# Kernel tuning notes

Measured on AMD Instinct MI355X. Metric: run time of the kernel, lower is better.

## Reference

```python
import jax, jax.numpy as jnp
import numpy as np

INPUT_SIZE = 128
HIDDEN = 256
BATCH = 64
SEQ = 2048


def setup_inputs() -> dict:
    key = jax.random.key(0)
    k1, k2, k3, k4, k5 = jax.random.split(key, 5)
    bound = 1.0 / np.sqrt(HIDDEN)
    x = jax.random.normal(k1, (BATCH, SEQ, INPUT_SIZE), dtype=jnp.float32)
    W_ih = jax.random.uniform(k2, (4 * HIDDEN, INPUT_SIZE), minval=-bound, maxval=bound, dtype=jnp.float32)
    W_hh = jax.random.uniform(k3, (4 * HIDDEN, HIDDEN), minval=-bound, maxval=bound, dtype=jnp.float32)
    b_ih = jax.random.uniform(k4, (4 * HIDDEN,), minval=-bound, maxval=bound, dtype=jnp.float32)
    b_hh = jax.random.uniform(k5, (4 * HIDDEN,), minval=-bound, maxval=bound, dtype=jnp.float32)
    return {"x": x, "W_ih": W_ih, "W_hh": W_hh, "b_ih": b_ih, "b_hh": b_hh}


def reference(x, W_ih, W_hh, b_ih, b_hh):
    # Faithful to the source: lstm_cell is called WITHOUT previous state at every
    # step, so h_prev = c_prev = 0 for each timestep. W_hh @ h_prev == 0, and
    # f_gate * c_prev == 0. Each timestep is independent -> vectorize over time.
    H = W_hh.shape[1]
    # gates: [B, T, 4H]
    gates = jnp.einsum('bti,gi->btg', x, W_ih) + b_ih + b_hh
    i_g, f_g, g_g, o_g = jnp.split(gates, 4, axis=-1)  # PyTorch order: i, f, g, o
    i_g = jax.nn.sigmoid(i_g)
    g_g = jnp.tanh(g_g)
    o_g = jax.nn.sigmoid(o_g)
    c = i_g * g_g                      # f_g * c_prev == 0 since c_prev = 0
    h = o_g * jnp.tanh(c)
    return (h, c)
```

## Files before the change

### kernel.cpp

```cpp
#include <hip/hip_runtime.h>
#include <hip/hip_bf16.h>
#include <stdint.h>


#define M_TOTAL   (64 * 2048)
#define K_DIM     128
#define N_OUT     256
#define TILE_ROWS 64
#define TILE_BYTES (TILE_ROWS * K_DIM * 4)
#define NBLK      256
#define ITERS     (M_TOTAL / TILE_ROWS / NBLK)

typedef __bf16 bf16x8 __attribute__((ext_vector_type(8)));
typedef float  f32x16 __attribute__((ext_vector_type(16)));

static __device__ __forceinline__ bf16x8 cvt8(float4 a, float4 b) {
    bf16x8 r;
    r[0] = (__bf16)a.x; r[1] = (__bf16)a.y; r[2] = (__bf16)a.z; r[3] = (__bf16)a.w;
    r[4] = (__bf16)b.x; r[5] = (__bf16)b.y; r[6] = (__bf16)b.z; r[7] = (__bf16)b.w;
    return r;
}

static __device__ __forceinline__ float fast_sigmoid(float x) {
    float e = __expf(-x);
    return __builtin_amdgcn_rcpf(1.0f + e);
}

static __device__ __forceinline__ float fast_tanh(float x) {
    float e = __expf(2.0f * x);
    return 1.0f - 2.0f * __builtin_amdgcn_rcpf(e + 1.0f);
}

static __device__ __forceinline__ void gload_lds16(const void* g, void* l) {
    __builtin_amdgcn_global_load_lds(
        (const __attribute__((address_space(1))) void*)g,
        (__attribute__((address_space(3))) void*)l, 16, 0, 0);
}

__global__ __launch_bounds__(512, 1)
void lstm_gates_kernel(const float* __restrict__ x,
                       const float* __restrict__ Wih,
                       const float* __restrict__ bih,
                       const float* __restrict__ bhh,
                       float* __restrict__ hout,
                       float* __restrict__ cout)
{
    __shared__ uint8_t lds[3 * TILE_BYTES];

    const int tid   = threadIdx.x;
    const int lane  = tid & 63;
    const int w     = tid >> 6;
    const int c0    = w * 32;
    const int ln31  = lane & 31;
    const int khalf = (lane >> 5) * 8;
    const uint32_t xr = (uint32_t)(ln31 & 7) << 4;

    bf16x8 bi[8], bg[8], bo[8];
    {
        const float4* wi = (const float4*)(Wih + (size_t)(0   + c0 + ln31) * K_DIM + khalf);
        const float4* wg = (const float4*)(Wih + (size_t)(512 + c0 + ln31) * K_DIM + khalf);
        const float4* wo = (const float4*)(Wih + (size_t)(768 + c0 + ln31) * K_DIM + khalf);
        #pragma unroll
        for (int kk = 0; kk < 8; ++kk) {
            bi[kk] = cvt8(wi[kk * 4], wi[kk * 4 + 1]);
            bg[kk] = cvt8(wg[kk * 4], wg[kk * 4 + 1]);
            bo[kk] = cvt8(wo[kk * 4], wo[kk * 4 + 1]);
        }
    }
    const float bias_i = bih[0   + c0 + ln31] + bhh[0   + c0 + ln31];
    const float bias_g = bih[512 + c0 + ln31] + bhh[512 + c0 + ln31];
    const float bias_o = bih[768 + c0 + ln31] + bhh[768 + c0 + ln31];

    const int t0 = blockIdx.x * ITERS;

    auto stage = [&](int buf, int t) {
        const uint8_t* gbase = (const uint8_t*)x + (size_t)t * TILE_BYTES;
        uint8_t* lbase = lds + (size_t)buf * TILE_BYTES + (size_t)w * 4096;
        #pragma unroll
        for (int j = 0; j < 4; ++j) {
            uint32_t d   = (uint32_t)w * 4096u + (uint32_t)j * 1024u + (uint32_t)lane * 16u;
            uint32_t src = d ^ (((d >> 9) & 7u) << 4);
            gload_lds16(gbase + src, lbase + (uint32_t)j * 1024u);
        }
    };

    auto compute = [&](int buf, int t) {
        const uint8_t* lbase = lds + (size_t)buf * TILE_BYTES;
        #pragma unroll
        for (int s = 0; s < 2; ++s) {
            const uint8_t* rowp = lbase + (uint32_t)(s * 32 + ln31) * 512u;
            bf16x8 a[8];
            #pragma unroll
            for (int kk = 0; kk < 8; ++kk) {
                const uint32_t off0 = (uint32_t)khalf * 4u + (uint32_t)kk * 64u;
                float4 lo = *(const float4*)(rowp + ((off0      ) ^ xr));
                float4 hi = *(const float4*)(rowp + ((off0 + 16u) ^ xr));
                a[kk] = cvt8(lo, hi);
            }
            f32x16 ai = (f32x16)0.0f, ag = (f32x16)0.0f, ao = (f32x16)0.0f;
            #pragma unroll
            for (int kk = 0; kk < 8; ++kk) {
                ai = __builtin_amdgcn_mfma_f32_32x32x16_bf16(a[kk], bi[kk], ai, 0, 0, 0);
                ag = __builtin_amdgcn_mfma_f32_32x32x16_bf16(a[kk], bg[kk], ag, 0, 0, 0);
                ao = __builtin_amdgcn_mfma_f32_32x32x16_bf16(a[kk], bo[kk], ao, 0, 0, 0);
            }
            const int m0 = t * TILE_ROWS + s * 32;
            #pragma unroll
            for (int r = 0; r < 16; ++r) {
                const int row = m0 + (r & 3) + 8 * (r >> 2) + 4 * (lane >> 5);
                float vi = ai[r] + bias_i;
                float vg = ag[r] + bias_g;
                float vo = ao[r] + bias_o;
                float si = fast_sigmoid(vi);
                float tg = fast_tanh(vg);
                float so = fast_sigmoid(vo);
                float c  = si * tg;
                float tc = fast_tanh(c);
                float h  = so * tc;
                const size_t off = (size_t)row * N_OUT + c0 + ln31;
                hout[off] = h;
                cout[off] = c;
            }
        }
    };

    stage(0, t0);
    for (int i = 0; i < ITERS; ++i) {
        __syncthreads();
        if (i + 1 < ITERS) stage((i + 1) % 3, t0 + i + 1);
        compute(i % 3, t0 + i);
    }
}

extern "C" void kernel_launch(void* const* d_in, const int* in_sizes, int n_in,
                              void* d_out, int out_size, void* d_ws, size_t ws_size,
                              hipStream_t stream) {
    const float* x   = (const float*)d_in[0];
    const float* Wih = (const float*)d_in[1];
    const float* bih = (const float*)d_in[3];
    const float* bhh = (const float*)d_in[4];
    float* hout = (float*)d_out;
    float* cout = hout + (size_t)M_TOTAL * N_OUT;

    lstm_gates_kernel<<<NBLK, 512, 0, stream>>>(x, Wih, bih, bhh, hout, cout);
}
```

Baseline: 341.7 us.

## Use 16x16 MFMA tiles with 1024-thread blocks and double-buffered LDS

Switches from 32x32x16 to 16x16x32 bf16 MFMA, so each of 16 waves now owns 16 output columns instead of 32. Block size doubles to 1024 threads, and the LDS ring drops from three buffers to two to fit the larger block. The aim is more resident waves to hide global-load and store latency, and smaller accumulators to cut register pressure. The cost is narrower 64-byte row segments per output store and less slack in the double-buffered pipeline.

```diff
diff --git a/kernel.cpp b/kernel.cpp
--- a/kernel.cpp
+++ b/kernel.cpp
@@ -12,7 +12,7 @@
 #define ITERS     (M_TOTAL / TILE_ROWS / NBLK)
 
 typedef __bf16 bf16x8 __attribute__((ext_vector_type(8)));
-typedef float  f32x16 __attribute__((ext_vector_type(16)));
+typedef float  f32x4  __attribute__((ext_vector_type(4)));
 
 static __device__ __forceinline__ bf16x8 cvt8(float4 a, float4 b) {
     bf16x8 r;
@@ -37,7 +37,7 @@
         (__attribute__((address_space(3))) void*)l, 16, 0, 0);
 }
 
-__global__ __launch_bounds__(512, 1)
+__global__ __launch_bounds__(1024, 4)
 void lstm_gates_kernel(const float* __restrict__ x,
                        const float* __restrict__ Wih,
                        const float* __restrict__ bih,
@@ -45,40 +45,39 @@
                        float* __restrict__ hout,
                        float* __restrict__ cout)
 {
-    __shared__ uint8_t lds[3 * TILE_BYTES];
+    __shared__ uint8_t lds[2 * TILE_BYTES];
 
-    const int tid   = threadIdx.x;
-    const int lane  = tid & 63;
-    const int w     = tid >> 6;
-    const int c0    = w * 32;
-    const int ln31  = lane & 31;
-    const int khalf = (lane >> 5) * 8;
-    const uint32_t xr = (uint32_t)(ln31 & 7) << 4;
+    const int tid  = threadIdx.x;
+    const int lane = tid & 63;
+    const int w    = tid >> 6;
+    const int c0   = w * 16;
+    const int r15  = lane & 15;
+    const int q    = lane >> 4;
 
-    bf16x8 bi[8], bg[8], bo[8];
+    bf16x8 bi[4], bg[4], bo[4];
     {
-        const float4* wi = (const float4*)(Wih + (size_t)(0   + c0 + ln31) * K_DIM + khalf);
-        const float4* wg = (const float4*)(Wih + (size_t)(512 + c0 + ln31) * K_DIM + khalf);
-        const float4* wo = (const float4*)(Wih + (size_t)(768 + c0 + ln31) * K_DIM + khalf);
+        const float* wi = Wih + (size_t)(0   + c0 + r15) * K_DIM + q * 8;
+        const float* wg = Wih + (size_t)(512 + c0 + r15) * K_DIM + q * 8;
+        const float* wo = Wih + (size_t)(768 + c0 + r15) * K_DIM + q * 8;
         #pragma unroll
-        for (int kk = 0; kk < 8; ++kk) {
-            bi[kk] = cvt8(wi[kk * 4], wi[kk * 4 + 1]);
-            bg[kk] = cvt8(wg[kk * 4], wg[kk * 4 + 1]);
-            bo[kk] = cvt8(wo[kk * 4], wo[kk * 4 + 1]);
+        for (int kk = 0; kk < 4; ++kk) {
+            bi[kk] = cvt8(*(const float4*)(wi + kk * 32), *(const float4*)(wi + kk * 32 + 4));
+            bg[kk] = cvt8(*(const float4*)(wg + kk * 32), *(const float4*)(wg + kk * 32 + 4));
+            bo[kk] = cvt8(*(const float4*)(wo + kk * 32), *(const float4*)(wo + kk * 32 + 4));
         }
     }
-    const float bias_i = bih[0   + c0 + ln31] + bhh[0   + c0 + ln31];
-    const float bias_g = bih[512 + c0 + ln31] + bhh[512 + c0 + ln31];
-    const float bias_o = bih[768 + c0 + ln31] + bhh[768 + c0 + ln31];
+    const float bias_i = bih[0   + c0 + r15] + bhh[0   + c0 + r15];
+    const float bias_g = bih[512 + c0 + r15] + bhh[512 + c0 + r15];
+    const float bias_o = bih[768 + c0 + r15] + bhh[768 + c0 + r15];
 
     const int t0 = blockIdx.x * ITERS;
 
     auto stage = [&](int buf, int t) {
         const uint8_t* gbase = (const uint8_t*)x + (size_t)t * TILE_BYTES;
-        uint8_t* lbase = lds + (size_t)buf * TILE_BYTES + (size_t)w * 4096;
+        uint8_t* lbase = lds + (size_t)buf * TILE_BYTES + (size_t)w * 2048;
         #pragma unroll
-        for (int j = 0; j < 4; ++j) {
-            uint32_t d   = (uint32_t)w * 4096u + (uint32_t)j * 1024u + (uint32_t)lane * 16u;
+        for (int j = 0; j < 2; ++j) {
+            uint32_t d   = (uint32_t)w * 2048u + (uint32_t)j * 1024u + (uint32_t)lane * 16u;
             uint32_t src = d ^ (((d >> 9) & 7u) << 4);
             gload_lds16(gbase + src, lbase + (uint32_t)j * 1024u);
         }
@@ -87,27 +86,29 @@
     auto compute = [&](int buf, int t) {
         const uint8_t* lbase = lds + (size_t)buf * TILE_BYTES;
         #pragma unroll
-        for (int s = 0; s < 2; ++s) {
-            const uint8_t* rowp = lbase + (uint32_t)(s * 32 + ln31) * 512u;
-            bf16x8 a[8];
+        for (int s = 0; s < 4; ++s) {
+            const uint32_t row = (uint32_t)(s * 16 + r15);
+            const uint8_t* rowp = lbase + row * 512u;
+            const uint32_t xr = (row & 7u) << 4;
+            bf16x8 a[4];
             #pragma unroll
-            for (int kk = 0; kk < 8; ++kk) {
-                const uint32_t off0 = (uint32_t)khalf * 4u + (uint32_t)kk * 64u;
-                float4 lo = *(const float4*)(rowp + ((off0      ) ^ xr));
-                float4 hi = *(const float4*)(rowp + ((off0 + 16u) ^ xr));
+            for (int kk = 0; kk < 4; ++kk) {
+                const uint32_t o = (uint32_t)kk * 128u + (uint32_t)q * 32u;
+                float4 lo = *(const float4*)(rowp + ((o       ) ^ xr));
+                float4 hi = *(const float4*)(rowp + ((o + 16u ) ^ xr));
                 a[kk] = cvt8(lo, hi);
             }
-            f32x16 ai = (f32x16)0.0f, ag = (f32x16)0.0f, ao = (f32x16)0.0f;
+            f32x4 ai = (f32x4)0.0f, ag = (f32x4)0.0f, ao = (f32x4)0.0f;
             #pragma unroll
-            for (int kk = 0; kk < 8; ++kk) {
-                ai = __builtin_amdgcn_mfma_f32_32x32x16_bf16(a[kk], bi[kk], ai, 0, 0, 0);
-                ag = __builtin_amdgcn_mfma_f32_32x32x16_bf16(a[kk], bg[kk], ag, 0, 0, 0);
-                ao = __builtin_amdgcn_mfma_f32_32x32x16_bf16(a[kk], bo[kk], ao, 0, 0, 0);
+            for (int kk = 0; kk < 4; ++kk) {
+                ai = __builtin_amdgcn_mfma_f32_16x16x32_bf16(a[kk], bi[kk], ai, 0, 0, 0);
+                ag = __builtin_amdgcn_mfma_f32_16x16x32_bf16(a[kk], bg[kk], ag, 0, 0, 0);
+                ao = __builtin_amdgcn_mfma_f32_16x16x32_bf16(a[kk], bo[kk], ao, 0, 0, 0);
             }
-            const int m0 = t * TILE_ROWS + s * 32;
+            const int m0 = t * TILE_ROWS + s * 16;
             #pragma unroll
-            for (int r = 0; r < 16; ++r) {
-                const int row = m0 + (r & 3) + 8 * (r >> 2) + 4 * (lane >> 5);
+            for (int r = 0; r < 4; ++r) {
+                const int rowo = m0 + q * 4 + r;
                 float vi = ai[r] + bias_i;
                 float vg = ag[r] + bias_g;
                 float vo = ao[r] + bias_o;
@@ -117,7 +118,7 @@
                 float c  = si * tg;
                 float tc = fast_tanh(c);
                 float h  = so * tc;
-                const size_t off = (size_t)row * N_OUT + c0 + ln31;
+                const size_t off = (size_t)rowo * N_OUT + c0 + r15;
                 hout[off] = h;
                 cout[off] = c;
             }
@@ -127,8 +128,8 @@
     stage(0, t0);
     for (int i = 0; i < ITERS; ++i) {
         __syncthreads();
-        if (i + 1 < ITERS) stage((i + 1) % 3, t0 + i + 1);
-        compute(i % 3, t0 + i);
+        if (i + 1 < ITERS) stage((i + 1) & 1, t0 + i + 1);
+        compute(i & 1, t0 + i);
     }
 }
 
@@ -142,5 +143,5 @@
     float* hout = (float*)d_out;
     float* cout = hout + (size_t)M_TOTAL * N_OUT;
 
-    lstm_gates_kernel<<<NBLK, 512, 0, stream>>>(x, Wih, bih, bhh, hout, cout);
+    lstm_gates_kernel<<<NBLK, 1024, 0, stream>>>(x, Wih, bih, bhh, hout, cout);
 }
```

New measurement: 340.4 us. No clear change (-0.4%).
